# Optimization experiments

Hardware: AMD Instinct MI355X
Metric: run time of the kernel (lower is better)

## Reference

```python
import jax, jax.numpy as jnp
from jax import lax
import numpy as np

B, T, NL = 512, 64, 32          # batch, timepoints per patient, n_labs
LAT, HID = 64, 128              # latent_dim, hidden_dim
SCALE, STEP, QPAD, TMAX = 365.0, 0.05, 2000, 2000


def setup_inputs() -> dict:
    key = jax.random.key(0)
    k = jax.random.split(key, 24)
    def rn(ki, shape, s=0.05):
        return jax.random.normal(ki, shape, jnp.float32) * s
    Din = 2 * NL + 1  # GRU input: labs, mask, dt
    return {
        "obs_vals": rn(k[0], (B, T, NL), 1.0),
        "age": jax.random.uniform(k[1], (B,), jnp.float32),
        "eps": rn(k[2], (B, LAT), 1.0),  # reparameterization noise (randn_like)
        "gru_Wih": rn(k[3], (Din, 3 * HID)), "gru_Whh": rn(k[4], (HID, 3 * HID)),
        "gru_bih": jnp.zeros((3 * HID,)), "gru_bhh": jnp.zeros((3 * HID,)),
        "Wmu": rn(k[5], (HID, LAT)), "bmu": jnp.zeros((LAT,)),
        "Wlv": rn(k[6], (HID, LAT)), "blv": jnp.zeros((LAT,)),
        "W1": rn(k[7], (LAT, HID)), "b1": jnp.zeros((HID,)),
        "W2": rn(k[8], (HID, HID)), "b2": jnp.zeros((HID,)),
        "W3": rn(k[9], (HID, LAT)), "b3": jnp.zeros((LAT,)),
        "Wo1": rn(k[10], (LAT, HID)), "bo1": jnp.zeros((HID,)),
        "Wo2": rn(k[11], (HID, NL)), "bo2": jnp.zeros((NL,)),
        "Ws1": rn(k[12], (LAT + 1, HID)), "bs1": jnp.zeros((HID,)),
        "Ws2": rn(k[13], (HID, 2)), "bs2": jnp.zeros((2,)),
        "obs_mask": jax.random.bernoulli(k[14], 0.7, (B, T, NL)),
        "timepoints": jnp.sort(jax.random.randint(k[15], (B, T), 0, TMAX), axis=1).astype(jnp.int32),
        "seq_lens": jax.random.randint(k[16], (B,), 1, T + 1).astype(jnp.int32),
    }


def reference(obs_vals, age, eps, gru_Wih, gru_Whh, gru_bih, gru_bhh,
              Wmu, bmu, Wlv, blv, W1, b1, W2, b2, W3, b3,
              Wo1, bo1, Wo2, bo2, Ws1, bs1, Ws2, bs2,
              obs_mask, timepoints, seq_lens):
    Bv, Tv, Dv = obs_vals.shape
    Hdim = gru_Whh.shape[0]
    tp = timepoints.astype(jnp.float32)

    # ---- RecognitionRNN (GRU over reversed sequence) ----
    dt = jnp.concatenate([jnp.zeros((Bv, 1)), tp[:, 1:] - tp[:, :-1]], axis=1)[..., None]
    maskf = obs_mask.astype(obs_vals.dtype)
    inp = jnp.concatenate([obs_vals * maskf, maskf, dt], axis=-1)  # [B,T,2*NL+1]
    x_seq = jnp.flip(inp, axis=1).transpose(1, 0, 2)  # [T,B,Din]

    def gru_step(h, x):
        gi = x @ gru_Wih + gru_bih
        gh = h @ gru_Whh + gru_bhh
        ir, iz, i_n = jnp.split(gi, 3, axis=-1)
        hr, hz, hn = jnp.split(gh, 3, axis=-1)
        r = jax.nn.sigmoid(ir + hr)
        zg = jax.nn.sigmoid(iz + hz)
        n = jnp.tanh(i_n + r * hn)
        h = (1.0 - zg) * n + zg * h
        return h, None

    h, _ = lax.scan(gru_step, jnp.zeros((Bv, Hdim), obs_vals.dtype), x_seq)
    mu = h @ Wmu + bmu
    logvar = h @ Wlv + blv
    z0 = mu + eps * jnp.exp(0.5 * logvar)  # reparameterize

    # ---- query times (padded unique; timepoints are >= 0 by construction) ----
    qd = jnp.unique(timepoints.reshape(-1), size=QPAD, fill_value=timepoints.max())
    query_t = qd.astype(jnp.float32) / SCALE  # [Q], nondecreasing

    # ---- torchdiffeq fixed-grid rk4 with step_size ----
    qnp = np.asarray(query_t)
    t0, t1 = float(qnp[0]), float(qnp[-1])
    niters = int(np.ceil((t1 - t0) / STEP + 1))
    grid = np.arange(niters) * STEP + t0
    if grid[-1] > t1:
        grid[-1] = t1
    grid = jnp.asarray(grid, jnp.float32)  # [G]

    def ode_f(z):
        return jnp.tanh(jnp.tanh(z @ W1 + b1) @ W2 + b2) @ W3 + b3

    def rk4_step(y, hstep):
        k1 = ode_f(y)
        k2 = ode_f(y + 0.5 * hstep * k1)
        k3 = ode_f(y + 0.5 * hstep * k2)
        k4 = ode_f(y + hstep * k3)
        y2 = y + (hstep / 6.0) * (k1 + 2.0 * k2 + 2.0 * k3 + k4)
        return y2, y2

    _, ys = lax.scan(rk4_step, z0, grid[1:] - grid[:-1])
    ys = jnp.concatenate([z0[None], ys], axis=0)  # [G,B,L]

    # linear interpolation of grid states at query_t (torchdiffeq behavior)
    gi = jnp.clip(jnp.searchsorted(grid, query_t, side="right") - 1, 0, grid.shape[0] - 2)
    tl, tr = grid[gi], grid[gi + 1]
    w = ((query_t - tl) / jnp.where(tr - tl == 0, 1.0, tr - tl))[:, None, None]
    z_traj = ys[gi] * (1.0 - w) + ys[gi + 1] * w  # [Q,B,L]

    # ---- reconstruction loss (vectorized over B,T) ----
    tq = tp / SCALE  # [B,T]
    idx_q = jnp.argmin(jnp.abs(query_t[None, None, :] - tq[:, :, None]), axis=-1)  # [B,T]
    z_bt = z_traj[idx_q, jnp.arange(Bv)[:, None]]  # [B,T,L]
    x_hat = jax.nn.relu(z_bt @ Wo1 + bo1) @ Wo2 + bo2  # [B,T,NL]
    valid = (jnp.arange(Tv)[None, :] < seq_lens[:, None]).astype(obs_vals.dtype)[..., None]
    m = maskf * valid
    n_obs = m.sum()
    recon = jnp.where(n_obs > 0,
                      (m * (x_hat - obs_vals) ** 2).sum() / jnp.maximum(n_obs, 1.0),
                      0.0)

    kl = -0.5 * jnp.mean(jnp.sum(1.0 + logvar - mu ** 2 - jnp.exp(logvar), axis=-1))

    # ---- z_eval at last observed timepoint per patient ----
    last_tp = jnp.take_along_axis(tp, (seq_lens - 1)[:, None], axis=1)[:, 0] / SCALE  # [B]
    idx_e = jnp.argmin(jnp.abs(query_t[None, :] - last_tp[:, None]), axis=-1)  # [B]
    z_eval = z_traj[idx_e, jnp.arange(Bv)]  # [B,L]
    log_hazard = jax.nn.relu(jnp.concatenate([z_eval, age[:, None]], axis=-1) @ Ws1 + bs1) @ Ws2 + bs2
    return log_hazard, recon, kl, z_eval
```

## Files before the change

### kernel.cpp

```cpp
#include <hip/hip_runtime.h>
#include <hip/hip_bf16.h>
#include <math.h>

#define B 512
#define T 64
#define NL 32
#define LAT 64
#define HID 128
#define DIN 65
#define G3 384
#define FSCALE 365.0f
#define MAXGRID 128

#define WS_MIN   0
#define WS_MAX   1
#define WS_NIT   2
#define WS_KL    3
#define WS_RE    4
#define WS_NO    5
#define WS_GRID  8
#define WS_Z0    (WS_GRID + MAXGRID)
#define WS_YS    (WS_Z0 + B*LAT)
#define WS_W31   (WS_YS + 120*B*LAT)
#define WS_B31   (WS_W31 + HID*HID)

typedef __attribute__((ext_vector_type(8))) __bf16 bf16x8;
typedef __attribute__((ext_vector_type(4))) float f32x4;

static __device__ __forceinline__ float tanh_fast(float x){
    float t = __builtin_amdgcn_exp2f(x * 2.8853900817779268f);
    return 1.0f - 2.0f * __builtin_amdgcn_rcpf(t + 1.0f);
}
static __device__ __forceinline__ float sigmoid_fast(float x){
    return __builtin_amdgcn_rcpf(1.0f + __builtin_amdgcn_exp2f(-1.4426950408889634f * x));
}
static __device__ __forceinline__ void bar_lds(){
    asm volatile("" ::: "memory");
    asm volatile("s_waitcnt lgkmcnt(0)" ::: "memory");
    __builtin_amdgcn_s_barrier();
    asm volatile("" ::: "memory");
}

__global__ void k_init(const int* __restrict__ tp, float* wsf){
    int* wsi = (int*)wsf;
    __shared__ int smin[256], smax[256];
    int tid = threadIdx.x;
    int mn = 2147483647, mx = -2147483647-1;
    for (int i = tid; i < B*T; i += 256){ int v = tp[i]; mn = min(mn,v); mx = max(mx,v); }
    smin[tid]=mn; smax[tid]=mx; __syncthreads();
    for (int s=128; s>0; s>>=1){
        if (tid<s){ smin[tid]=min(smin[tid],smin[tid+s]); smax[tid]=max(smax[tid],smax[tid+s]); }
        __syncthreads();
    }
    if (tid==0){
        wsi[WS_MIN]=smin[0]; wsi[WS_MAX]=smax[0];
        wsf[WS_KL]=0.f; wsf[WS_RE]=0.f; wsf[WS_NO]=0.f;
    }
}

__global__ void k_grid(float* wsf){
    int* wsi=(int*)wsf;
    float t0f = (float)wsi[WS_MIN] / FSCALE;
    float t1f = (float)wsi[WS_MAX] / FSCALE;
    double t0d = (double)t0f, t1d = (double)t1f;
    int nit = (int)ceil((t1d-t0d)/0.05 + 1.0);
    if (nit < 1) nit = 1;
    if (nit > MAXGRID) nit = MAXGRID;
    if (threadIdx.x==0) wsi[WS_NIT] = nit;
    int k = threadIdx.x;
    if (k < nit){
        double g = (double)k * 0.05 + t0d;
        if (k == nit-1 && g > t1d) g = t1d;
        wsf[WS_GRID + k] = (float)g;
    }
}

__global__ __launch_bounds__(256) void k_w31(
    const float* __restrict__ W1, const float* __restrict__ W3,
    const float* __restrict__ b3, float* wsf)
{
    int gid = blockIdx.x*256 + threadIdx.x;
    int k = gid >> 5, n0 = (gid & 31)*4;
    float4 acc = {0.f,0.f,0.f,0.f};
    #pragma unroll 8
    for (int l=0;l<64;++l){
        float w3v = W3[k*LAT + l];
        float4 w1v = *(const float4*)&W1[l*HID + n0];
        acc.x = fmaf(w3v, w1v.x, acc.x);
        acc.y = fmaf(w3v, w1v.y, acc.y);
        acc.z = fmaf(w3v, w1v.z, acc.z);
        acc.w = fmaf(w3v, w1v.w, acc.w);
    }
    *(float4*)&wsf[WS_W31 + k*HID + n0] = acc;
    if (blockIdx.x==0 && threadIdx.x < HID){
        int n = threadIdx.x; float a = 0.f;
        #pragma unroll 8
        for (int l=0;l<64;++l) a = fmaf(b3[l], W1[l*HID+n], a);
        wsf[WS_B31 + n] = a;
    }
}

__global__ __launch_bounds__(512) void k_gru(
    const float* __restrict__ obs, const float* __restrict__ eps,
    const float* __restrict__ Wih, const float* __restrict__ Whh,
    const float* __restrict__ bih, const float* __restrict__ bhh,
    const float* __restrict__ Wmu, const float* __restrict__ bmu,
    const float* __restrict__ Wlv, const float* __restrict__ blv,
    const int* __restrict__ maskI, const int* __restrict__ tp,
    float* wsf)
{
    const int b0 = blockIdx.x * 16;
    const int tid = threadIdx.x;
    const int w = tid >> 6, lane = tid & 63;
    const int g = lane >> 4, c = lane & 15;
    const int xr = tid >> 5, xl = tid & 31;

    __shared__ __align__(16) __bf16 xh[16][232];
    __shared__ int   tps[16][64];
    __shared__ float dts[16];
    __shared__ float lvs[16][64];
    __shared__ float red[8];

    ((int2*)tps)[tid] = ((const int2*)(tp + (size_t)b0*T))[tid];
    {
        unsigned* xz = (unsigned*)&xh[0][0];
        #pragma unroll
        for (int i=0;i<1856;i+=512) xz[i+tid] = 0u;
    }

    bf16x8 wr[6], wz[6], wi[2], wh[4];
    #pragma unroll
    for (int q=0;q<6;++q){
        int kt = q<2 ? q : q+1;
        #pragma unroll
        for (int e=0;e<8;++e){
            int k = kt*32 + g*8 + e;
            float vr, vz;
            if (k < 64){ vr = Wih[k*G3 + 16*w+c];      vz = Wih[k*G3 + 128+16*w+c]; }
            else       { vr = Whh[(k-96)*G3 + 16*w+c]; vz = Whh[(k-96)*G3 + 128+16*w+c]; }
            wr[q][e] = (__bf16)vr; wz[q][e] = (__bf16)vz;
        }
    }
    #pragma unroll
    for (int q=0;q<2;++q)
        #pragma unroll
        for (int e=0;e<8;++e)
            wi[q][e] = (__bf16)Wih[(q*32+g*8+e)*G3 + 256+16*w+c];
    #pragma unroll
    for (int q=0;q<4;++q)
        #pragma unroll
        for (int e=0;e<8;++e)
            wh[q][e] = (__bf16)Whh[(q*32+g*8+e)*G3 + 256+16*w+c];
    const float wdr = Wih[64*G3 + 16*w+c];
    const float wdz = Wih[64*G3 + 128+16*w+c];
    const float wdn = Wih[64*G3 + 256+16*w+c];
    const float rb  = bih[16*w+c]     + bhh[16*w+c];
    const float zb  = bih[128+16*w+c] + bhh[128+16*w+c];
    const float inb = bih[256+16*w+c];
    const float hnb = bhh[256+16*w+c];

    __syncthreads();

    {
        float mv = (float)maskI[((size_t)(b0+xr)*T + 63)*NL + xl];
        float ov = obs[((size_t)(b0+xr)*T + 63)*NL + xl];
        xh[xr][xl]    = (__bf16)(ov*mv);
        xh[xr][32+xl] = (__bf16)mv;
        if (xl==0) dts[xr] = (float)(tps[xr][63]-tps[xr][62]);
    }
    float ovP = 0.f, mvP = 0.f;
    {
        mvP = (float)maskI[((size_t)(b0+xr)*T + 62)*NL + xl];
        ovP = obs[((size_t)(b0+xr)*T + 62)*NL + xl];
    }

    float hold[4] = {0.f,0.f,0.f,0.f};

    for (int s=0;s<T;++s){
        bar_lds();
        bf16x8 A0 = *(const bf16x8*)&xh[c][0*32 + g*8];
        bf16x8 A1 = *(const bf16x8*)&xh[c][1*32 + g*8];
        bf16x8 A2 = *(const bf16x8*)&xh[c][3*32 + g*8];
        bf16x8 A3 = *(const bf16x8*)&xh[c][4*32 + g*8];
        bf16x8 A4 = *(const bf16x8*)&xh[c][5*32 + g*8];
        bf16x8 A5 = *(const bf16x8*)&xh[c][6*32 + g*8];
        const float dt0=dts[4*g], dt1=dts[4*g+1], dt2=dts[4*g+2], dt3=dts[4*g+3];
        float ovN=0.f, mvN=0.f; const int t2 = 61-s;
        if (t2 >= 0){
            mvN = (float)maskI[((size_t)(b0+xr)*T + t2)*NL + xl];
            ovN = obs[((size_t)(b0+xr)*T + t2)*NL + xl];
        }
        f32x4 racc={0,0,0,0}, zacc={0,0,0,0}, inacc={0,0,0,0}, hnacc={0,0,0,0};
        racc  = __builtin_amdgcn_mfma_f32_16x16x32_bf16(A0, wr[0], racc, 0,0,0);
        zacc  = __builtin_amdgcn_mfma_f32_16x16x32_bf16(A0, wz[0], zacc, 0,0,0);
        inacc = __builtin_amdgcn_mfma_f32_16x16x32_bf16(A0, wi[0], inacc,0,0,0);
        hnacc = __builtin_amdgcn_mfma_f32_16x16x32_bf16(A2, wh[0], hnacc,0,0,0);
        racc  = __builtin_amdgcn_mfma_f32_16x16x32_bf16(A1, wr[1], racc, 0,0,0);
        zacc  = __builtin_amdgcn_mfma_f32_16x16x32_bf16(A1, wz[1], zacc, 0,0,0);
        inacc = __builtin_amdgcn_mfma_f32_16x16x32_bf16(A1, wi[1], inacc,0,0,0);
        hnacc = __builtin_amdgcn_mfma_f32_16x16x32_bf16(A3, wh[1], hnacc,0,0,0);
        racc  = __builtin_amdgcn_mfma_f32_16x16x32_bf16(A2, wr[2], racc, 0,0,0);
        zacc  = __builtin_amdgcn_mfma_f32_16x16x32_bf16(A2, wz[2], zacc, 0,0,0);
        hnacc = __builtin_amdgcn_mfma_f32_16x16x32_bf16(A4, wh[2], hnacc,0,0,0);
        racc  = __builtin_amdgcn_mfma_f32_16x16x32_bf16(A3, wr[3], racc, 0,0,0);
        zacc  = __builtin_amdgcn_mfma_f32_16x16x32_bf16(A3, wz[3], zacc, 0,0,0);
        hnacc = __builtin_amdgcn_mfma_f32_16x16x32_bf16(A5, wh[3], hnacc,0,0,0);
        racc  = __builtin_amdgcn_mfma_f32_16x16x32_bf16(A4, wr[4], racc, 0,0,0);
        zacc  = __builtin_amdgcn_mfma_f32_16x16x32_bf16(A4, wz[4], zacc, 0,0,0);
        racc  = __builtin_amdgcn_mfma_f32_16x16x32_bf16(A5, wr[5], racc, 0,0,0);
        zacc  = __builtin_amdgcn_mfma_f32_16x16x32_bf16(A5, wz[5], zacc, 0,0,0);
        float hnew[4]; const float dtv[4] = {dt0,dt1,dt2,dt3};
        #pragma unroll
        for (int j=0;j<4;++j){
            float dv = dtv[j];
            float r  = sigmoid_fast(racc[j] + rb + dv*wdr);
            float zg = sigmoid_fast(zacc[j] + zb + dv*wdz);
            float n  = tanh_fast(inacc[j] + inb + dv*wdn + r*(hnacc[j] + hnb));
            float hv = (1.f - zg)*n + zg*hold[j];
            hold[j] = hv; hnew[j] = hv;
        }
        bar_lds();
        #pragma unroll
        for (int j=0;j<4;++j) xh[4*g+j][96+16*w+c] = (__bf16)hnew[j];
        if (s < T-1){
            const int tn = 62 - s;
            xh[xr][xl]    = (__bf16)(ovP*mvP);
            xh[xr][32+xl] = (__bf16)mvP;
            if (xl==0) dts[xr] = (tn>0) ? (float)(tps[xr][tn]-tps[xr][tn-1]) : 0.f;
        }
        ovP = ovN; mvP = mvN;
    }
    __syncthreads();

    const int col4 = 16*(w&3)+c;
    bf16x8 Ah0 = *(const bf16x8*)&xh[c][96+0*32+g*8];
    bf16x8 Ah1 = *(const bf16x8*)&xh[c][96+1*32+g*8];
    bf16x8 Ah2 = *(const bf16x8*)&xh[c][96+2*32+g*8];
    bf16x8 Ah3 = *(const bf16x8*)&xh[c][96+3*32+g*8];
    const float* Wm = (w<4)? Wmu : Wlv;
    f32x4 acc={0,0,0,0};
    {
        bf16x8 bf0,bf1,bf2,bf3;
        #pragma unroll
        for (int e=0;e<8;++e){
            bf0[e] = (__bf16)Wm[(0*32+g*8+e)*LAT + col4];
            bf1[e] = (__bf16)Wm[(1*32+g*8+e)*LAT + col4];
            bf2[e] = (__bf16)Wm[(2*32+g*8+e)*LAT + col4];
            bf3[e] = (__bf16)Wm[(3*32+g*8+e)*LAT + col4];
        }
        acc = __builtin_amdgcn_mfma_f32_16x16x32_bf16(Ah0, bf0, acc, 0,0,0);
        acc = __builtin_amdgcn_mfma_f32_16x16x32_bf16(Ah1, bf1, acc, 0,0,0);
        acc = __builtin_amdgcn_mfma_f32_16x16x32_bf16(Ah2, bf2, acc, 0,0,0);
        acc = __builtin_amdgcn_mfma_f32_16x16x32_bf16(Ah3, bf3, acc, 0,0,0);
    }
    const float mbias = (w<4)? bmu[col4] : blv[col4];
    if (w>=4){
        #pragma unroll
        for (int j=0;j<4;++j) lvs[4*g+j][col4] = acc[j] + mbias;
    }
    __syncthreads();
    if (w<4){
        float kl = 0.f;
        #pragma unroll
        for (int j=0;j<4;++j){
            float mu = acc[j] + mbias;
            float lv = lvs[4*g+j][col4];
            int row = b0 + 4*g + j;
            float z0 = mu + eps[(size_t)row*LAT + col4]*expf(0.5f*lv);
            wsf[WS_Z0 + (size_t)row*LAT + col4] = z0;
            wsf[WS_YS + (size_t)row*LAT + col4] = z0;
            kl += 1.f + lv - mu*mu - expf(lv);
        }
        #pragma unroll
        for (int off=32; off>0; off>>=1) kl += __shfl_xor(kl, off);
        if (lane==0) red[w] = kl;
    }
    __syncthreads();
    if (tid==0) atomicAdd(&wsf[WS_KL], red[0]+red[1]+red[2]+red[3]);
}

__global__ __launch_bounds__(512) void k_ode(
    const float* __restrict__ W1, const float* __restrict__ b1,
    const float* __restrict__ W2, const float* __restrict__ b2,
    const float* __restrict__ W3, const float* __restrict__ b3,
    float* wsf)
{
    const int b0 = blockIdx.x * 16;
    const int tid = threadIdx.x;
    const int w = tid >> 6, lane = tid & 63;
    const int g = lane >> 4, c = lane & 15;
    const int hc = 16*w + c;
    const int lc = 16*(w&3) + c;
    const int* wsi = (const int*)wsf;
    const int nit = wsi[WS_NIT];

    __shared__ __align__(16) __bf16 Gl[16][136];
    __shared__ __align__(16) __bf16 Hl[16][136];
    __shared__ float gls[MAXGRID];

    bf16x8 w2f[4], w31f[4], w3f[4];
    #pragma unroll
    for (int q=0;q<4;++q)
        #pragma unroll
        for (int e=0;e<8;++e){
            w2f[q][e]  = (__bf16)W2[(q*32+g*8+e)*HID + hc];
            w31f[q][e] = (__bf16)wsf[WS_W31 + (q*32+g*8+e)*HID + hc];
            w3f[q][e]  = (__bf16)W3[(q*32+g*8+e)*LAT + lc];
        }
    const float b1v  = b1[hc];
    const float b2v  = b2[hc];
    const float b31v = wsf[WS_B31 + hc];
    const float b3v  = b3[lc];

    for (int kk=tid; kk<MAXGRID; kk+=512) gls[kk]=wsf[WS_GRID+kk];

    {
        int r = tid >> 5, l0 = (tid & 31)*2;
        float2 zv = *(const float2*)&wsf[WS_Z0 + (size_t)(b0+r)*LAT + l0];
        Gl[r][l0]   = (__bf16)zv.x;
        Gl[r][l0+1] = (__bf16)zv.y;
    }
    float y[4];
    #pragma unroll
    for (int j=0;j<4;++j)
        y[j] = wsf[WS_Z0 + (size_t)(b0+4*g+j)*LAT + lc];
    __syncthreads();

    f32x4 U;
    {
        bf16x8 az0 = *(const bf16x8*)&Gl[c][g*8];
        bf16x8 az1 = *(const bf16x8*)&Gl[c][32+g*8];
        bf16x8 wf0, wf1;
        #pragma unroll
        for (int e=0;e<8;++e){
            wf0[e] = (__bf16)W1[(g*8+e)*HID + hc];
            wf1[e] = (__bf16)W1[(32+g*8+e)*HID + hc];
        }
        f32x4 a = {0.f,0.f,0.f,0.f};
        a = __builtin_amdgcn_mfma_f32_16x16x32_bf16(az0, wf0, a, 0,0,0);
        a = __builtin_amdgcn_mfma_f32_16x16x32_bf16(az1, wf1, a, 0,0,0);
        U = a;
    }
    __syncthreads();

    #pragma unroll
    for (int j=0;j<4;++j)
        Gl[4*g+j][hc] = (__bf16)tanh_fast(U[j] + b1v);
    __syncthreads();

    f32x4 Uacc={0,0,0,0}, faccv={0,0,0,0};

    for (int i=0; i<nit-1; ++i){
        const float h = gls[i+1]-gls[i];
        #pragma unroll
        for (int sub=0; sub<4; ++sub){
            {
                bf16x8 a0 = *(const bf16x8*)&Gl[c][g*8];
                bf16x8 a1 = *(const bf16x8*)&Gl[c][32+g*8];
                bf16x8 a2 = *(const bf16x8*)&Gl[c][64+g*8];
                bf16x8 a3 = *(const bf16x8*)&Gl[c][96+g*8];
                f32x4 ca={0,0,0,0}, cb={0,0,0,0};
                ca = __builtin_amdgcn_mfma_f32_16x16x32_bf16(a0, w2f[0], ca, 0,0,0);
                cb = __builtin_amdgcn_mfma_f32_16x16x32_bf16(a2, w2f[2], cb, 0,0,0);
                ca = __builtin_amdgcn_mfma_f32_16x16x32_bf16(a1, w2f[1], ca, 0,0,0);
                cb = __builtin_amdgcn_mfma_f32_16x16x32_bf16(a3, w2f[3], cb, 0,0,0);
                #pragma unroll
                for (int j=0;j<4;++j)
                    Hl[4*g+j][hc] = (__bf16)tanh_fast(ca[j]+cb[j]+b2v);
            }
            bar_lds();
            {
                bf16x8 h0 = *(const bf16x8*)&Hl[c][g*8];
                bf16x8 h1 = *(const bf16x8*)&Hl[c][32+g*8];
                bf16x8 h2 = *(const bf16x8*)&Hl[c][64+g*8];
                bf16x8 h3 = *(const bf16x8*)&Hl[c][96+g*8];
                f32x4 va={0,0,0,0}, vb={0,0,0,0};
                va = __builtin_amdgcn_mfma_f32_16x16x32_bf16(h0, w31f[0], va, 0,0,0);
                vb = __builtin_amdgcn_mfma_f32_16x16x32_bf16(h2, w31f[2], vb, 0,0,0);
                va = __builtin_amdgcn_mfma_f32_16x16x32_bf16(h1, w31f[1], va, 0,0,0);
                vb = __builtin_amdgcn_mfma_f32_16x16x32_bf16(h3, w31f[3], vb, 0,0,0);
                f32x4 V;
                #pragma unroll
                for (int j=0;j<4;++j) V[j] = va[j] + vb[j] + b31v;

                f32x4 fv = {0,0,0,0};
                if (w < 4){
                    f32x4 fa={0,0,0,0}, fb={0,0,0,0};
                    fa = __builtin_amdgcn_mfma_f32_16x16x32_bf16(h0, w3f[0], fa, 0,0,0);
                    fb = __builtin_amdgcn_mfma_f32_16x16x32_bf16(h2, w3f[2], fb, 0,0,0);
                    fa = __builtin_amdgcn_mfma_f32_16x16x32_bf16(h1, w3f[1], fa, 0,0,0);
                    fb = __builtin_amdgcn_mfma_f32_16x16x32_bf16(h3, w3f[3], fb, 0,0,0);
                    #pragma unroll
                    for (int j=0;j<4;++j) fv[j] = fa[j] + fb[j] + b3v;
                }
                if (sub==0){ Uacc = V; faccv = fv; }
                else if (sub==3){ Uacc += V; faccv += fv; }
                else { Uacc += 2.f*V; faccv += 2.f*fv; }

                if (sub < 3){
                    const float al = (sub==2) ? h : 0.5f*h;
                    #pragma unroll
                    for (int j=0;j<4;++j)
                        Gl[4*g+j][hc] = (__bf16)tanh_fast(fmaf(al, V[j], U[j]) + b1v);
                } else {
                    const float h6 = h*(1.0f/6.0f);
                    if (w < 4){
                        #pragma unroll
                        for (int j=0;j<4;++j){
                            y[j] = fmaf(h6, faccv[j], y[j]);
                            wsf[WS_YS + ((size_t)(i+1)*B + (b0+4*g+j))*LAT + lc] = y[j];
                        }
                    }
                    #pragma unroll
                    for (int j=0;j<4;++j){
                        U[j] = fmaf(h6, Uacc[j], U[j]);
                        Gl[4*g+j][hc] = (__bf16)tanh_fast(U[j] + b1v);
                    }
                }
            }
            bar_lds();
        }
    }
}

__global__ __launch_bounds__(512) void k_recon(
    const float* __restrict__ obs, const int* __restrict__ maskI,
    const int* __restrict__ tp, const int* __restrict__ seq,
    const float* __restrict__ Wo1, const float* __restrict__ bo1,
    const float* __restrict__ Wo2, const float* __restrict__ bo2,
    float* wsf)
{
    const int b = blockIdx.x, tid = threadIdx.x;
    const int w = tid >> 6, lane = tid & 63;
    const int g = lane >> 4, c = lane & 15;
    __shared__ __align__(16) __bf16 zbt[64][72];
    __shared__ __align__(16) __bf16 hb[64][136];
    __shared__ float gls[MAXGRID];
    __shared__ float red[16];
    const int* wsi=(const int*)wsf;
    const int nit = wsi[WS_NIT];
    for (int i=tid;i<MAXGRID;i+=512) gls[i]=wsf[WS_GRID+i];

    bf16x8 wo1f[2], wo2f[4];
    #pragma unroll
    for (int q=0;q<2;++q)
        #pragma unroll
        for (int e=0;e<8;++e)
            wo1f[q][e] = (__bf16)Wo1[(q*32+g*8+e)*HID + 16*w+c];
    {
        int n = w & 1;
        #pragma unroll
        for (int q=0;q<4;++q)
            #pragma unroll
            for (int e=0;e<8;++e)
                wo2f[q][e] = (__bf16)Wo2[(q*32+g*8+e)*NL + 16*n+c];
    }
    const float bo1v = bo1[16*w+c];
    const float bo2v = bo2[16*(w&1)+c];
    const int sl = seq[b];
    __syncthreads();

    {
        int t = tid >> 3, seg = tid & 7;
        float tq = (float)tp[b*T+t] / FSCALE;
        int lo=0, hi=nit;
        while (lo<hi){ int mid=(lo+hi)>>1; if (gls[mid]<=tq) lo=mid+1; else hi=mid; }
        int k = lo-1; if (k<0) k=0; if (nit>=2 && k>nit-2) k=nit-2; if (nit<2) k=0;
        float wq=0.f;
        if (nit>=2){ float tl=gls[k], tr=gls[k+1]; float den=(tr-tl==0.f)?1.f:(tr-tl); wq=(tq-tl)/den; }
        size_t o0 = (size_t)WS_YS + ((size_t)k*B + b)*LAT + seg*8;
        float4 za0 = *(const float4*)&wsf[o0];
        float4 za1 = *(const float4*)&wsf[o0+4];
        float4 zb0, zb1;
        if (nit>=2){
            zb0 = *(const float4*)&wsf[o0 + (size_t)B*LAT];
            zb1 = *(const float4*)&wsf[o0 + (size_t)B*LAT + 4];
        } else { zb0 = za0; zb1 = za1; }
        __bf16* dst = &zbt[t][seg*8];
        dst[0] = (__bf16)(za0.x*(1.f-wq)+zb0.x*wq);
        dst[1] = (__bf16)(za0.y*(1.f-wq)+zb0.y*wq);
        dst[2] = (__bf16)(za0.z*(1.f-wq)+zb0.z*wq);
        dst[3] = (__bf16)(za0.w*(1.f-wq)+zb0.w*wq);
        dst[4] = (__bf16)(za1.x*(1.f-wq)+zb1.x*wq);
        dst[5] = (__bf16)(za1.y*(1.f-wq)+zb1.y*wq);
        dst[6] = (__bf16)(za1.z*(1.f-wq)+zb1.z*wq);
        dst[7] = (__bf16)(za1.w*(1.f-wq)+zb1.w*wq);
    }
    __syncthreads();

    #pragma unroll
    for (int m=0;m<4;++m){
        f32x4 acc = {0.f,0.f,0.f,0.f};
        bf16x8 a0 = *(const bf16x8*)&zbt[16*m+c][g*8];
        bf16x8 a1 = *(const bf16x8*)&zbt[16*m+c][32+g*8];
        acc = __builtin_amdgcn_mfma_f32_16x16x32_bf16(a0, wo1f[0], acc, 0,0,0);
        acc = __builtin_amdgcn_mfma_f32_16x16x32_bf16(a1, wo1f[1], acc, 0,0,0);
        #pragma unroll
        for (int j=0;j<4;++j)
            hb[16*m+4*g+j][16*w+c] = (__bf16)fmaxf(acc[j] + bo1v, 0.f);
    }
    __syncthreads();

    float esum = 0.f, ncnt = 0.f;
    {
        int m = w >> 1, n = w & 1;
        f32x4 ca = {0.f,0.f,0.f,0.f}, cb = {0.f,0.f,0.f,0.f};
        bf16x8 a0 = *(const bf16x8*)&hb[16*m+c][g*8];
        bf16x8 a1 = *(const bf16x8*)&hb[16*m+c][32+g*8];
        bf16x8 a2 = *(const bf16x8*)&hb[16*m+c][64+g*8];
        bf16x8 a3 = *(const bf16x8*)&hb[16*m+c][96+g*8];
        ca = __builtin_amdgcn_mfma_f32_16x16x32_bf16(a0, wo2f[0], ca, 0,0,0);
        cb = __builtin_amdgcn_mfma_f32_16x16x32_bf16(a2, wo2f[2], cb, 0,0,0);
        ca = __builtin_amdgcn_mfma_f32_16x16x32_bf16(a1, wo2f[1], ca, 0,0,0);
        cb = __builtin_amdgcn_mfma_f32_16x16x32_bf16(a3, wo2f[3], cb, 0,0,0);
        #pragma unroll
        for (int j=0;j<4;++j){
            int t = 16*m + 4*g + j;
            int col = 16*n + c;
            float xh2 = (ca[j]+cb[j]) + bo2v;
            float mv = (float)maskI[(b*T+t)*NL+col] * ((t<sl)?1.f:0.f);
            float d = xh2 - obs[(b*T+t)*NL+col];
            esum = fmaf(mv*d, d, esum);
            ncnt += mv;
        }
    }
    #pragma unroll
    for (int off=32; off>0; off>>=1){
        esum += __shfl_xor(esum, off);
        ncnt += __shfl_xor(ncnt, off);
    }
    if (lane==0){ red[w] = esum; red[8+w] = ncnt; }
    __syncthreads();
    if (tid==0){
        float s=0.f, nn=0.f;
        #pragma unroll
        for (int i=0;i<8;++i){ s += red[i]; nn += red[8+i]; }
        atomicAdd(&wsf[WS_RE], s);
        atomicAdd(&wsf[WS_NO], nn);
    }
}

__global__ __launch_bounds__(128) void k_surv(
    const float* __restrict__ age, const int* __restrict__ tp, const int* __restrict__ seq,
    const float* __restrict__ Ws1, const float* __restrict__ bs1,
    const float* __restrict__ Ws2, const float* __restrict__ bs2,
    float* wsf, float* out)
{
    int b=blockIdx.x, tid=threadIdx.x;
    __shared__ float gls[MAXGRID];
    __shared__ float ze[64];
    __shared__ float pred[4];
    const int* wsi=(const int*)wsf; int nit=wsi[WS_NIT];
    for (int i=tid;i<MAXGRID;i+=128) gls[i]=wsf[WS_GRID+i];
    __syncthreads();
    int sl = seq[b];
    float tq = (float)tp[b*T + sl-1] / FSCALE;
    int lo=0,hi=nit;
    while(lo<hi){int mid=(lo+hi)>>1; if (gls[mid]<=tq) lo=mid+1; else hi=mid;}
    int k=lo-1; if(k<0)k=0; if(nit>=2 && k>nit-2)k=nit-2; if (nit<2) k=0;
    float w=0.f;
    if (nit>=2){ float tl=gls[k],tr=gls[k+1]; float den=(tr-tl==0.f)?1.f:(tr-tl); w=(tq-tl)/den; }
    if (tid<LAT){
        size_t o0 = (size_t)WS_YS + ((size_t)k*B+b)*LAT+tid;
        float zl = wsf[o0]*(1.f-w) + ((nit>=2)? wsf[o0+(size_t)B*LAT]*w : 0.f);
        ze[tid]=zl;
        out[1026 + b*LAT + tid] = zl;
    }
    __syncthreads();
    float hj = bs1[tid];
    #pragma unroll 8
    for (int l=0;l<LAT;++l) hj = fmaf(ze[l], Ws1[l*HID+tid], hj);
    hj = fmaf(age[b], Ws1[LAT*HID+tid], hj);
    hj = fmaxf(hj,0.f);
    float p0 = hj*Ws2[tid*2+0], p1 = hj*Ws2[tid*2+1];
    #pragma unroll
    for (int off=32;off>0;off>>=1){ p0 += __shfl_down(p0,off); p1 += __shfl_down(p1,off); }
    int wv = tid>>6;
    if ((tid&63)==0){ pred[wv*2]=p0; pred[wv*2+1]=p1; }
    __syncthreads();
    if (tid==0){
        out[b*2+0] = bs2[0] + pred[0]+pred[2];
        out[b*2+1] = bs2[1] + pred[1]+pred[3];
    }
}

__global__ void k_fin(float* wsf, float* out){
    float n = wsf[WS_NO];
    out[1024] = (n>0.f) ? (wsf[WS_RE]/fmaxf(n,1.f)) : 0.f;
    out[1025] = -0.5f * (wsf[WS_KL] / (float)B);
}

extern "C" void kernel_launch(void* const* d_in, const int* in_sizes, int n_in,
                              void* d_out, int out_size, void* d_ws, size_t ws_size,
                              hipStream_t stream) {
    const float* obs   = (const float*)d_in[0];
    const float* age   = (const float*)d_in[1];
    const float* eps   = (const float*)d_in[2];
    const float* Wih   = (const float*)d_in[3];
    const float* Whh   = (const float*)d_in[4];
    const float* bih   = (const float*)d_in[5];
    const float* bhh   = (const float*)d_in[6];
    const float* Wmu   = (const float*)d_in[7];
    const float* bmu   = (const float*)d_in[8];
    const float* Wlv   = (const float*)d_in[9];
    const float* blv   = (const float*)d_in[10];
    const float* W1    = (const float*)d_in[11];
    const float* b1    = (const float*)d_in[12];
    const float* W2    = (const float*)d_in[13];
    const float* b2    = (const float*)d_in[14];
    const float* W3    = (const float*)d_in[15];
    const float* b3    = (const float*)d_in[16];
    const float* Wo1   = (const float*)d_in[17];
    const float* bo1   = (const float*)d_in[18];
    const float* Wo2   = (const float*)d_in[19];
    const float* bo2   = (const float*)d_in[20];
    const float* Ws1   = (const float*)d_in[21];
    const float* bs1   = (const float*)d_in[22];
    const float* Ws2   = (const float*)d_in[23];
    const float* bs2   = (const float*)d_in[24];
    const int*   maskI = (const int*)d_in[25];
    const int*   tp    = (const int*)d_in[26];
    const int*   seq   = (const int*)d_in[27];
    float* wsf = (float*)d_ws;
    float* out = (float*)d_out;

    k_init<<<1, 256, 0, stream>>>(tp, wsf);
    k_grid<<<1, 128, 0, stream>>>(wsf);
    k_w31<<<16, 256, 0, stream>>>(W1, W3, b3, wsf);
    k_gru<<<B/16, 512, 0, stream>>>(obs, eps, Wih, Whh, bih, bhh, Wmu, bmu, Wlv, blv,
                                    maskI, tp, wsf);
    k_ode<<<B/16, 512, 0, stream>>>(W1, b1, W2, b2, W3, b3, wsf);
    k_recon<<<B, 512, 0, stream>>>(obs, maskI, tp, seq, Wo1, bo1, Wo2, bo2, wsf);
    k_surv<<<B, 128, 0, stream>>>(age, tp, seq, Ws1, bs1, Ws2, bs2, wsf, out);
    k_fin<<<1, 1, 0, stream>>>(wsf, out);
}
```

Measured before the change: 524.6 us.

## Swizzle LDS tiles, raise MFMA priority, and fuse small setup/survival kernels

Applies an XOR swizzle to the LDS row layout in the GRU and ODE kernels to reduce bank conflicts on the bf16x8 A-operand reads. Wraps the MFMA blocks in the ODE kernel with s_setprio so the matrix work gets issue priority. Merges k_init with k_grid and k_surv with k_recon, removing two kernel launches and their launch gaps. The swizzle adds address arithmetic on every LDS access, and the fused survival step runs inside the 512-thread recon blocks, where only part of the threads are active.

```diff
diff --git a/kernel.cpp b/kernel.cpp
--- a/kernel.cpp
+++ b/kernel.cpp
@@ -27,6 +27,8 @@
 typedef __attribute__((ext_vector_type(8))) __bf16 bf16x8;
 typedef __attribute__((ext_vector_type(4))) float f32x4;
 
+#define SWZ(row) ((((row)>>3)&1)<<5)
+
 static __device__ __forceinline__ float tanh_fast(float x){
     float t = __builtin_amdgcn_exp2f(x * 2.8853900817779268f);
     return 1.0f - 2.0f * __builtin_amdgcn_rcpf(t + 1.0f);
@@ -41,7 +43,7 @@
     asm volatile("" ::: "memory");
 }
 
-__global__ void k_init(const int* __restrict__ tp, float* wsf){
+__global__ void k_setup(const int* __restrict__ tp, float* wsf){
     int* wsi = (int*)wsf;
     __shared__ int smin[256], smax[256];
     int tid = threadIdx.x;
@@ -52,26 +54,20 @@
         if (tid<s){ smin[tid]=min(smin[tid],smin[tid+s]); smax[tid]=max(smax[tid],smax[tid+s]); }
         __syncthreads();
     }
-    if (tid==0){
-        wsi[WS_MIN]=smin[0]; wsi[WS_MAX]=smax[0];
-        wsf[WS_KL]=0.f; wsf[WS_RE]=0.f; wsf[WS_NO]=0.f;
-    }
-}
-
-__global__ void k_grid(float* wsf){
-    int* wsi=(int*)wsf;
-    float t0f = (float)wsi[WS_MIN] / FSCALE;
-    float t1f = (float)wsi[WS_MAX] / FSCALE;
+    float t0f = (float)smin[0] / FSCALE;
+    float t1f = (float)smax[0] / FSCALE;
     double t0d = (double)t0f, t1d = (double)t1f;
     int nit = (int)ceil((t1d-t0d)/0.05 + 1.0);
     if (nit < 1) nit = 1;
     if (nit > MAXGRID) nit = MAXGRID;
-    if (threadIdx.x==0) wsi[WS_NIT] = nit;
-    int k = threadIdx.x;
-    if (k < nit){
-        double g = (double)k * 0.05 + t0d;
-        if (k == nit-1 && g > t1d) g = t1d;
-        wsf[WS_GRID + k] = (float)g;
+    if (tid==0){
+        wsi[WS_NIT] = nit;
+        wsf[WS_KL]=0.f; wsf[WS_RE]=0.f; wsf[WS_NO]=0.f;
+    }
+    if (tid < nit){
+        double g = (double)tid * 0.05 + t0d;
+        if (tid == nit-1 && g > t1d) g = t1d;
+        wsf[WS_GRID + tid] = (float)g;
     }
 }
 
@@ -120,10 +116,13 @@
     __shared__ float dts[16];
     __shared__ float lvs[16][64];
     __shared__ float red[8];
+    char* xbase = (char*)&xh[0][0];
+    #define XH_RD(row, bytecol) (*(const bf16x8*)(xbase + (row)*464 + ((bytecol) ^ SWZ(row))))
+    #define XH_WPTR(row, bytecol) ((__bf16*)(xbase + (row)*464 + ((bytecol) ^ SWZ(row))))
 
     ((int2*)tps)[tid] = ((const int2*)(tp + (size_t)b0*T))[tid];
     {
-        unsigned* xz = (unsigned*)&xh[0][0];
+        unsigned* xz = (unsigned*)xbase;
         #pragma unroll
         for (int i=0;i<1856;i+=512) xz[i+tid] = 0u;
     }
@@ -164,8 +163,8 @@
     {
         float mv = (float)maskI[((size_t)(b0+xr)*T + 63)*NL + xl];
         float ov = obs[((size_t)(b0+xr)*T + 63)*NL + xl];
-        xh[xr][xl]    = (__bf16)(ov*mv);
-        xh[xr][32+xl] = (__bf16)mv;
+        *XH_WPTR(xr, 2*xl)      = (__bf16)(ov*mv);
+        *XH_WPTR(xr, 64 + 2*xl) = (__bf16)mv;
         if (xl==0) dts[xr] = (float)(tps[xr][63]-tps[xr][62]);
     }
     float ovP = 0.f, mvP = 0.f;
@@ -178,12 +177,12 @@
 
     for (int s=0;s<T;++s){
         bar_lds();
-        bf16x8 A0 = *(const bf16x8*)&xh[c][0*32 + g*8];
-        bf16x8 A1 = *(const bf16x8*)&xh[c][1*32 + g*8];
-        bf16x8 A2 = *(const bf16x8*)&xh[c][3*32 + g*8];
-        bf16x8 A3 = *(const bf16x8*)&xh[c][4*32 + g*8];
-        bf16x8 A4 = *(const bf16x8*)&xh[c][5*32 + g*8];
-        bf16x8 A5 = *(const bf16x8*)&xh[c][6*32 + g*8];
+        bf16x8 A0 = XH_RD(c, 0   + 16*g);
+        bf16x8 A1 = XH_RD(c, 64  + 16*g);
+        bf16x8 A2 = XH_RD(c, 192 + 16*g);
+        bf16x8 A3 = XH_RD(c, 256 + 16*g);
+        bf16x8 A4 = XH_RD(c, 320 + 16*g);
+        bf16x8 A5 = XH_RD(c, 384 + 16*g);
         const float dt0=dts[4*g], dt1=dts[4*g+1], dt2=dts[4*g+2], dt3=dts[4*g+3];
         float ovN=0.f, mvN=0.f; const int t2 = 61-s;
         if (t2 >= 0){
@@ -221,11 +220,12 @@
         }
         bar_lds();
         #pragma unroll
-        for (int j=0;j<4;++j) xh[4*g+j][96+16*w+c] = (__bf16)hnew[j];
+        for (int j=0;j<4;++j)
+            *XH_WPTR(4*g+j, 192 + 2*(16*w+c)) = (__bf16)hnew[j];
         if (s < T-1){
             const int tn = 62 - s;
-            xh[xr][xl]    = (__bf16)(ovP*mvP);
-            xh[xr][32+xl] = (__bf16)mvP;
+            *XH_WPTR(xr, 2*xl)      = (__bf16)(ovP*mvP);
+            *XH_WPTR(xr, 64 + 2*xl) = (__bf16)mvP;
             if (xl==0) dts[xr] = (tn>0) ? (float)(tps[xr][tn]-tps[xr][tn-1]) : 0.f;
         }
         ovP = ovN; mvP = mvN;
@@ -233,10 +233,10 @@
     __syncthreads();
 
     const int col4 = 16*(w&3)+c;
-    bf16x8 Ah0 = *(const bf16x8*)&xh[c][96+0*32+g*8];
-    bf16x8 Ah1 = *(const bf16x8*)&xh[c][96+1*32+g*8];
-    bf16x8 Ah2 = *(const bf16x8*)&xh[c][96+2*32+g*8];
-    bf16x8 Ah3 = *(const bf16x8*)&xh[c][96+3*32+g*8];
+    bf16x8 Ah0 = XH_RD(c, 192 + 0   + 16*g);
+    bf16x8 Ah1 = XH_RD(c, 192 + 64  + 16*g);
+    bf16x8 Ah2 = XH_RD(c, 192 + 128 + 16*g);
+    bf16x8 Ah3 = XH_RD(c, 192 + 192 + 16*g);
     const float* Wm = (w<4)? Wmu : Wlv;
     f32x4 acc={0,0,0,0};
     {
@@ -277,6 +277,8 @@
     }
     __syncthreads();
     if (tid==0) atomicAdd(&wsf[WS_KL], red[0]+red[1]+red[2]+red[3]);
+    #undef XH_RD
+    #undef XH_WPTR
 }
 
 __global__ __launch_bounds__(512) void k_ode(
@@ -297,6 +299,10 @@
     __shared__ __align__(16) __bf16 Gl[16][136];
     __shared__ __align__(16) __bf16 Hl[16][136];
     __shared__ float gls[MAXGRID];
+    char* gbase = (char*)&Gl[0][0];
+    char* hbase = (char*)&Hl[0][0];
+    #define LDS_RD(base, row, bytecol) (*(const bf16x8*)((base) + (row)*272 + ((bytecol) ^ SWZ(row))))
+    #define LDS_WPTR(base, row, bytecol) ((__bf16*)((base) + (row)*272 + ((bytecol) ^ SWZ(row))))
 
     bf16x8 w2f[4], w31f[4], w3f[4];
     #pragma unroll
@@ -317,8 +323,9 @@
     {
         int r = tid >> 5, l0 = (tid & 31)*2;
         float2 zv = *(const float2*)&wsf[WS_Z0 + (size_t)(b0+r)*LAT + l0];
-        Gl[r][l0]   = (__bf16)zv.x;
-        Gl[r][l0+1] = (__bf16)zv.y;
+        __bf16* p = LDS_WPTR(gbase, r, 2*l0);
+        p[0] = (__bf16)zv.x;
+        p[1] = (__bf16)zv.y;
     }
     float y[4];
     #pragma unroll
@@ -328,8 +335,8 @@
 
     f32x4 U;
     {
-        bf16x8 az0 = *(const bf16x8*)&Gl[c][g*8];
-        bf16x8 az1 = *(const bf16x8*)&Gl[c][32+g*8];
+        bf16x8 az0 = LDS_RD(gbase, c, 16*g);
+        bf16x8 az1 = LDS_RD(gbase, c, 64 + 16*g);
         bf16x8 wf0, wf1;
         #pragma unroll
         for (int e=0;e<8;++e){
@@ -345,7 +352,7 @@
 
     #pragma unroll
     for (int j=0;j<4;++j)
-        Gl[4*g+j][hc] = (__bf16)tanh_fast(U[j] + b1v);
+        *LDS_WPTR(gbase, 4*g+j, 2*hc) = (__bf16)tanh_fast(U[j] + b1v);
     __syncthreads();
 
     f32x4 Uacc={0,0,0,0}, faccv={0,0,0,0};
@@ -355,34 +362,33 @@
         #pragma unroll
         for (int sub=0; sub<4; ++sub){
             {
-                bf16x8 a0 = *(const bf16x8*)&Gl[c][g*8];
-                bf16x8 a1 = *(const bf16x8*)&Gl[c][32+g*8];
-                bf16x8 a2 = *(const bf16x8*)&Gl[c][64+g*8];
-                bf16x8 a3 = *(const bf16x8*)&Gl[c][96+g*8];
+                bf16x8 a0 = LDS_RD(gbase, c, 0   + 16*g);
+                bf16x8 a1 = LDS_RD(gbase, c, 64  + 16*g);
+                bf16x8 a2 = LDS_RD(gbase, c, 128 + 16*g);
+                bf16x8 a3 = LDS_RD(gbase, c, 192 + 16*g);
+                __builtin_amdgcn_s_setprio(1);
                 f32x4 ca={0,0,0,0}, cb={0,0,0,0};
                 ca = __builtin_amdgcn_mfma_f32_16x16x32_bf16(a0, w2f[0], ca, 0,0,0);
                 cb = __builtin_amdgcn_mfma_f32_16x16x32_bf16(a2, w2f[2], cb, 0,0,0);
                 ca = __builtin_amdgcn_mfma_f32_16x16x32_bf16(a1, w2f[1], ca, 0,0,0);
                 cb = __builtin_amdgcn_mfma_f32_16x16x32_bf16(a3, w2f[3], cb, 0,0,0);
+                __builtin_amdgcn_s_setprio(0);
                 #pragma unroll
                 for (int j=0;j<4;++j)
-                    Hl[4*g+j][hc] = (__bf16)tanh_fast(ca[j]+cb[j]+b2v);
+                    *LDS_WPTR(hbase, 4*g+j, 2*hc) = (__bf16)tanh_fast(ca[j]+cb[j]+b2v);
             }
             bar_lds();
             {
-                bf16x8 h0 = *(const bf16x8*)&Hl[c][g*8];
-                bf16x8 h1 = *(const bf16x8*)&Hl[c][32+g*8];
-                bf16x8 h2 = *(const bf16x8*)&Hl[c][64+g*8];
-                bf16x8 h3 = *(const bf16x8*)&Hl[c][96+g*8];
+                bf16x8 h0 = LDS_RD(hbase, c, 0   + 16*g);
+                bf16x8 h1 = LDS_RD(hbase, c, 64  + 16*g);
+                bf16x8 h2 = LDS_RD(hbase, c, 128 + 16*g);
+                bf16x8 h3 = LDS_RD(hbase, c, 192 + 16*g);
+                __builtin_amdgcn_s_setprio(1);
                 f32x4 va={0,0,0,0}, vb={0,0,0,0};
                 va = __builtin_amdgcn_mfma_f32_16x16x32_bf16(h0, w31f[0], va, 0,0,0);
                 vb = __builtin_amdgcn_mfma_f32_16x16x32_bf16(h2, w31f[2], vb, 0,0,0);
                 va = __builtin_amdgcn_mfma_f32_16x16x32_bf16(h1, w31f[1], va, 0,0,0);
                 vb = __builtin_amdgcn_mfma_f32_16x16x32_bf16(h3, w31f[3], vb, 0,0,0);
-                f32x4 V;
-                #pragma unroll
-                for (int j=0;j<4;++j) V[j] = va[j] + vb[j] + b31v;
-
                 f32x4 fv = {0,0,0,0};
                 if (w < 4){
                     f32x4 fa={0,0,0,0}, fb={0,0,0,0};
@@ -393,6 +399,11 @@
                     #pragma unroll
                     for (int j=0;j<4;++j) fv[j] = fa[j] + fb[j] + b3v;
                 }
+                __builtin_amdgcn_s_setprio(0);
+                f32x4 V;
+                #pragma unroll
+                for (int j=0;j<4;++j) V[j] = va[j] + vb[j] + b31v;
+
                 if (sub==0){ Uacc = V; faccv = fv; }
                 else if (sub==3){ Uacc += V; faccv += fv; }
                 else { Uacc += 2.f*V; faccv += 2.f*fv; }
@@ -401,7 +412,7 @@
                     const float al = (sub==2) ? h : 0.5f*h;
                     #pragma unroll
                     for (int j=0;j<4;++j)
-                        Gl[4*g+j][hc] = (__bf16)tanh_fast(fmaf(al, V[j], U[j]) + b1v);
+                        *LDS_WPTR(gbase, 4*g+j, 2*hc) = (__bf16)tanh_fast(fmaf(al, V[j], U[j]) + b1v);
                 } else {
                     const float h6 = h*(1.0f/6.0f);
                     if (w < 4){
@@ -414,13 +425,15 @@
                     #pragma unroll
                     for (int j=0;j<4;++j){
                         U[j] = fmaf(h6, Uacc[j], U[j]);
-                        Gl[4*g+j][hc] = (__bf16)tanh_fast(U[j] + b1v);
+                        *LDS_WPTR(gbase, 4*g+j, 2*hc) = (__bf16)tanh_fast(U[j] + b1v);
                     }
                 }
             }
             bar_lds();
         }
     }
+    #undef LDS_RD
+    #undef LDS_WPTR
 }
 
 __global__ __launch_bounds__(512) void k_recon(
@@ -428,7 +441,10 @@
     const int* __restrict__ tp, const int* __restrict__ seq,
     const float* __restrict__ Wo1, const float* __restrict__ bo1,
     const float* __restrict__ Wo2, const float* __restrict__ bo2,
-    float* wsf)
+    const float* __restrict__ age,
+    const float* __restrict__ Ws1, const float* __restrict__ bs1,
+    const float* __restrict__ Ws2, const float* __restrict__ bs2,
+    float* wsf, float* out)
 {
     const int b = blockIdx.x, tid = threadIdx.x;
     const int w = tid >> 6, lane = tid & 63;
@@ -437,6 +453,8 @@
     __shared__ __align__(16) __bf16 hb[64][136];
     __shared__ float gls[MAXGRID];
     __shared__ float red[16];
+    __shared__ float ze[64];
+    __shared__ float pred[4];
     const int* wsi=(const int*)wsf;
     const int nit = wsi[WS_NIT];
     for (int i=tid;i<MAXGRID;i+=512) gls[i]=wsf[WS_GRID+i];
@@ -538,49 +556,38 @@
         atomicAdd(&wsf[WS_RE], s);
         atomicAdd(&wsf[WS_NO], nn);
     }
-}
-
-__global__ __launch_bounds__(128) void k_surv(
-    const float* __restrict__ age, const int* __restrict__ tp, const int* __restrict__ seq,
-    const float* __restrict__ Ws1, const float* __restrict__ bs1,
-    const float* __restrict__ Ws2, const float* __restrict__ bs2,
-    float* wsf, float* out)
-{
-    int b=blockIdx.x, tid=threadIdx.x;
-    __shared__ float gls[MAXGRID];
-    __shared__ float ze[64];
-    __shared__ float pred[4];
-    const int* wsi=(const int*)wsf; int nit=wsi[WS_NIT];
-    for (int i=tid;i<MAXGRID;i+=128) gls[i]=wsf[WS_GRID+i];
-    __syncthreads();
-    int sl = seq[b];
-    float tq = (float)tp[b*T + sl-1] / FSCALE;
-    int lo=0,hi=nit;
-    while(lo<hi){int mid=(lo+hi)>>1; if (gls[mid]<=tq) lo=mid+1; else hi=mid;}
-    int k=lo-1; if(k<0)k=0; if(nit>=2 && k>nit-2)k=nit-2; if (nit<2) k=0;
-    float w=0.f;
-    if (nit>=2){ float tl=gls[k],tr=gls[k+1]; float den=(tr-tl==0.f)?1.f:(tr-tl); w=(tq-tl)/den; }
-    if (tid<LAT){
-        size_t o0 = (size_t)WS_YS + ((size_t)k*B+b)*LAT+tid;
-        float zl = wsf[o0]*(1.f-w) + ((nit>=2)? wsf[o0+(size_t)B*LAT]*w : 0.f);
-        ze[tid]=zl;
-        out[1026 + b*LAT + tid] = zl;
-    }
-    __syncthreads();
-    float hj = bs1[tid];
-    #pragma unroll 8
-    for (int l=0;l<LAT;++l) hj = fmaf(ze[l], Ws1[l*HID+tid], hj);
-    hj = fmaf(age[b], Ws1[LAT*HID+tid], hj);
-    hj = fmaxf(hj,0.f);
-    float p0 = hj*Ws2[tid*2+0], p1 = hj*Ws2[tid*2+1];
-    #pragma unroll
-    for (int off=32;off>0;off>>=1){ p0 += __shfl_down(p0,off); p1 += __shfl_down(p1,off); }
-    int wv = tid>>6;
-    if ((tid&63)==0){ pred[wv*2]=p0; pred[wv*2+1]=p1; }
-    __syncthreads();
-    if (tid==0){
-        out[b*2+0] = bs2[0] + pred[0]+pred[2];
-        out[b*2+1] = bs2[1] + pred[1]+pred[3];
+
+    {
+        float tq = (float)tp[b*T + sl-1] / FSCALE;
+        int lo=0,hi=nit;
+        while(lo<hi){int mid=(lo+hi)>>1; if (gls[mid]<=tq) lo=mid+1; else hi=mid;}
+        int k=lo-1; if(k<0)k=0; if(nit>=2 && k>nit-2)k=nit-2; if (nit<2) k=0;
+        float wq=0.f;
+        if (nit>=2){ float tl=gls[k],tr=gls[k+1]; float den=(tr-tl==0.f)?1.f:(tr-tl); wq=(tq-tl)/den; }
+        if (tid<LAT){
+            size_t o0 = (size_t)WS_YS + ((size_t)k*B+b)*LAT+tid;
+            float zl = wsf[o0]*(1.f-wq) + ((nit>=2)? wsf[o0+(size_t)B*LAT]*wq : 0.f);
+            ze[tid]=zl;
+            out[1026 + b*LAT + tid] = zl;
+        }
+        __syncthreads();
+        if (tid < 128){
+            float hj = bs1[tid];
+            #pragma unroll 8
+            for (int l=0;l<LAT;++l) hj = fmaf(ze[l], Ws1[l*HID+tid], hj);
+            hj = fmaf(age[b], Ws1[LAT*HID+tid], hj);
+            hj = fmaxf(hj,0.f);
+            float p0 = hj*Ws2[tid*2+0], p1 = hj*Ws2[tid*2+1];
+            #pragma unroll
+            for (int off=32;off>0;off>>=1){ p0 += __shfl_down(p0,off); p1 += __shfl_down(p1,off); }
+            int wv = tid>>6;
+            if ((tid&63)==0){ pred[wv*2]=p0; pred[wv*2+1]=p1; }
+        }
+        __syncthreads();
+        if (tid==0){
+            out[b*2+0] = bs2[0] + pred[0]+pred[2];
+            out[b*2+1] = bs2[1] + pred[1]+pred[3];
+        }
     }
 }
 
@@ -624,13 +631,12 @@
     float* wsf = (float*)d_ws;
     float* out = (float*)d_out;
 
-    k_init<<<1, 256, 0, stream>>>(tp, wsf);
-    k_grid<<<1, 128, 0, stream>>>(wsf);
+    k_setup<<<1, 256, 0, stream>>>(tp, wsf);
     k_w31<<<16, 256, 0, stream>>>(W1, W3, b3, wsf);
     k_gru<<<B/16, 512, 0, stream>>>(obs, eps, Wih, Whh, bih, bhh, Wmu, bmu, Wlv, blv,
                                     maskI, tp, wsf);
     k_ode<<<B/16, 512, 0, stream>>>(W1, b1, W2, b2, W3, b3, wsf);
-    k_recon<<<B, 512, 0, stream>>>(obs, maskI, tp, seq, Wo1, bo1, Wo2, bo2, wsf);
-    k_surv<<<B, 128, 0, stream>>>(age, tp, seq, Ws1, bs1, Ws2, bs2, wsf, out);
+    k_recon<<<B, 512, 0, stream>>>(obs, maskI, tp, seq, Wo1, bo1, Wo2, bo2,
+                                   age, Ws1, bs1, Ws2, bs2, wsf, out);
     k_fin<<<1, 1, 0, stream>>>(wsf, out);
 }
```

New measurement: 527.8 us. About the same (+0.6%).
